# Optimization experiments

Hardware: AMD Instinct MI355X
Metric: run time of the kernel (lower is better)

Reference implementation:

```python
import jax, jax.numpy as jnp
import numpy as np
from jax import lax

B, T, D = 64, 1024, 256   # batch, seq_len, input_size
H, C = 1024, 1000         # hidden_size, num_classes


def setup_inputs() -> dict:
    key = jax.random.key(0)
    k_x, k_ih, k_hh, k_b, k_fc, k_fb = jax.random.split(key, 6)
    x = jax.random.normal(k_x, (B, T, D), dtype=jnp.float32)
    # scaled init so the 1024-step recurrence stays numerically sane
    w_ih = jax.random.normal(k_ih, (H, D), dtype=jnp.float32) * (1.0 / np.sqrt(D))
    w_hh = jax.random.normal(k_hh, (H, H), dtype=jnp.float32) * (0.5 / np.sqrt(H))
    b_mod = jax.random.normal(k_b, (H,), dtype=jnp.float32) * 0.01 - 0.1
    w_fc = jax.random.normal(k_fc, (C, H), dtype=jnp.float32) * (1.0 / np.sqrt(H))
    b_fc = jnp.zeros((C,), dtype=jnp.float32)
    return {"x": x, "w_ih": w_ih, "w_hh": w_hh, "b_mod": b_mod,
            "w_fc": w_fc, "b_fc": b_fc}


def reference(x, w_ih, w_hh, b_mod, w_fc, b_fc):
    # modReLU RNN: h_t = sign(z_t) * relu(|z_t| + b),  z_t = W_ih x_t + W_hh h_{t-1}
    # fc head applied to last hidden state (out[:, -1, :]).
    bsz = x.shape[0]
    # precompute input projections for all timesteps: [B, T, H]
    xproj = jnp.einsum('btd,hd->bth', x, w_ih)

    def step(h, x_t):
        z = x_t + h @ w_hh.T                      # [B, H]
        h_new = jnp.sign(z) * jnp.maximum(jnp.abs(z) + b_mod, 0.0)
        return h_new, None

    h0 = jnp.zeros((bsz, w_hh.shape[0]), dtype=x.dtype)
    h_last, _ = lax.scan(step, h0, jnp.swapaxes(xproj, 0, 1))  # scan over T
    return h_last @ w_fc.T + b_fc  # [B, C]
```

## Files before the change

kernel.cpp:

```cpp
#include <hip/hip_runtime.h>

typedef __bf16 bf16;
typedef __bf16 bf16x4 __attribute__((ext_vector_type(4)));
typedef __bf16 bf16x8 __attribute__((ext_vector_type(8)));
typedef float f32x4 __attribute__((ext_vector_type(4)));
typedef int   i32x4 __attribute__((ext_vector_type(4)));
typedef unsigned long long u64;
typedef unsigned int u32;

#define T_STEPS 1024
#define BATCH   64
#define DIN     256
#define HID     1024
#define NBLK    32
#define RING    8
#define SENT    0x7F7F7F7Fu

__global__ __launch_bounds__(256) void xproj_gemm(
    const float* __restrict__ x, const float* __restrict__ w_ih,
    bf16* __restrict__ xproj)
{
    __shared__ bf16 As[128 * 40];
    __shared__ bf16 Bs[128 * 40];
    const int tid = threadIdx.x;
    const int m0 = blockIdx.x * 128;
    const int n0 = blockIdx.y * 128;
    const int w = tid >> 6, lane = tid & 63;
    const int r = lane & 15, q = lane >> 4;

    f32x4 acc[2][8];
    #pragma unroll
    for (int i = 0; i < 2; i++)
        #pragma unroll
        for (int j = 0; j < 8; j++)
            acc[i][j] = (f32x4){0.f, 0.f, 0.f, 0.f};

    for (int kk = 0; kk < 8; kk++) {
        const int k0 = kk * 32;
        __syncthreads();
        #pragma unroll
        for (int j = 0; j < 4; j++) {
            int u = tid + j * 256;
            int row = u >> 3, c4 = u & 7;
            float4 fa = *(const float4*)&x[(size_t)(m0 + row) * DIN + k0 + c4 * 4];
            bf16x4 va = { (bf16)fa.x, (bf16)fa.y, (bf16)fa.z, (bf16)fa.w };
            *(bf16x4*)&As[row * 40 + c4 * 4] = va;
            float4 fb = *(const float4*)&w_ih[(size_t)(n0 + row) * DIN + k0 + c4 * 4];
            bf16x4 vb = { (bf16)fb.x, (bf16)fb.y, (bf16)fb.z, (bf16)fb.w };
            *(bf16x4*)&Bs[row * 40 + c4 * 4] = vb;
        }
        __syncthreads();
        bf16x8 a0 = *(const bf16x8*)&As[(w * 32 + r) * 40 + q * 8];
        bf16x8 a1 = *(const bf16x8*)&As[(w * 32 + 16 + r) * 40 + q * 8];
        #pragma unroll
        for (int nt = 0; nt < 8; nt++) {
            bf16x8 bb = *(const bf16x8*)&Bs[(nt * 16 + r) * 40 + q * 8];
            acc[0][nt] = __builtin_amdgcn_mfma_f32_16x16x32_bf16(a0, bb, acc[0][nt], 0, 0, 0);
            acc[1][nt] = __builtin_amdgcn_mfma_f32_16x16x32_bf16(a1, bb, acc[1][nt], 0, 0, 0);
        }
    }

    #pragma unroll
    for (int mi = 0; mi < 2; mi++)
        #pragma unroll
        for (int nt = 0; nt < 8; nt++)
            #pragma unroll
            for (int reg = 0; reg < 4; reg++) {
                int gm = m0 + w * 32 + mi * 16 + q * 4 + reg;
                int n  = n0 + nt * 16 + r;
                int b  = gm >> 10, t = gm & 1023;
                xproj[(((t << 6) + b) << 10) + n] = (bf16)acc[mi][nt][reg];
            }
}

__global__ __launch_bounds__(512, 2) void rnn_rec(
    const float* __restrict__ w_hh, const float* __restrict__ b_mod,
    const bf16* __restrict__ xproj, u64* __restrict__ hbuf,
    float* __restrict__ hT)
{
    __shared__ bf16 Wl[64 * 1032];
    __shared__ float Red[24 * 272];

    const int tid = threadIdx.x;
    const int fg2 = (int)(blockIdx.x >> 1);
    const int half = (int)(blockIdx.x & 1);
    const int f0 = fg2 * 64;
    const int b0 = half * 32;
    const int w = tid >> 6, lane = tid & 63;
    const int r = lane & 15, q = lane >> 4;
    const int bg = w & 1, kq = w >> 1;
    const int batchA = b0 + bg * 16 + r;

    for (int j = 0; j < 32; j++) {
        int u = tid + j * 512;
        int row = u >> 8, c4 = u & 255;
        float4 f = *(const float4*)&w_hh[(size_t)(f0 + row) * HID + c4 * 4];
        bf16x4 v = { (bf16)f.x, (bf16)f.y, (bf16)f.z, (bf16)f.w };
        *(bf16x4*)&Wl[row * 1032 + c4 * 4] = v;
    }
    const int myF = f0 + kq * 16 + r;
    const float bc = b_mod[myF];
    __syncthreads();

    bf16x8 Bf[4][8];
    #pragma unroll
    for (int nt = 0; nt < 4; nt++)
        #pragma unroll
        for (int ks = 0; ks < 8; ks++)
            Bf[nt][ks] = *(const bf16x8*)&Wl[(nt * 16 + r) * 1032 + kq * 256 + ks * 32 + q * 8];

    u32* hbuf32 = (u32*)hbuf;
    const size_t fragOff = (size_t)batchA * 2048 + kq * 512 + q * 16;

    float xpv[4];
    #pragma unroll
    for (int reg = 0; reg < 4; reg++) {
        int b = b0 + bg * 16 + q * 4 + reg;
        xpv[reg] = (float)xproj[(b << 10) + myF];
    }

    for (int t = 0; t < T_STEPS; t++) {
        const int rp = t & (RING - 1), wp = (t + 1) & (RING - 1);
        const char* Hb = (const char*)hbuf + (size_t)rp * 131072 + fragOff;

        union { i32x4 v[8]; u32 wd[32]; bf16x8 f[8]; } A;
        for (;;) {
            asm volatile(
                "global_load_dwordx4 %0, %8, off sc0 sc1\n\t"
                "global_load_dwordx4 %1, %8, off offset:64 sc0 sc1\n\t"
                "global_load_dwordx4 %2, %8, off offset:128 sc0 sc1\n\t"
                "global_load_dwordx4 %3, %8, off offset:192 sc0 sc1\n\t"
                "global_load_dwordx4 %4, %8, off offset:256 sc0 sc1\n\t"
                "global_load_dwordx4 %5, %8, off offset:320 sc0 sc1\n\t"
                "global_load_dwordx4 %6, %8, off offset:384 sc0 sc1\n\t"
                "global_load_dwordx4 %7, %8, off offset:448 sc0 sc1\n\t"
                "s_waitcnt vmcnt(0)"
                : "=v"(A.v[0]), "=v"(A.v[1]), "=v"(A.v[2]), "=v"(A.v[3]),
                  "=v"(A.v[4]), "=v"(A.v[5]), "=v"(A.v[6]), "=v"(A.v[7])
                : "v"(Hb)
                : "memory");
            bool ok = true;
            #pragma unroll
            for (int i = 0; i < 32; i++) ok &= (A.wd[i] != SENT);
            if (__all((int)ok)) break;
        }

        f32x4 acc[4];
        #pragma unroll
        for (int nt = 0; nt < 4; nt++) acc[nt] = (f32x4){0.f,0.f,0.f,0.f};
        #pragma unroll
        for (int ks = 0; ks < 8; ks++)
            #pragma unroll
            for (int nt = 0; nt < 4; nt++)
                acc[nt] = __builtin_amdgcn_mfma_f32_16x16x32_bf16(A.f[ks], Bf[nt][ks], acc[nt], 0, 0, 0);

        #pragma unroll
        for (int nt = 0; nt < 4; nt++) {
            if (nt == kq) continue;
            const int s = (kq - nt - 1) & 3;
            const int base = ((bg * 4 + nt) * 3 + s) * 272;
            #pragma unroll
            for (int reg = 0; reg < 4; reg++)
                Red[base + (q * 4 + reg) * 17 + r] = acc[nt][reg];
        }
        __syncthreads();

        float hv4[4];
        #pragma unroll
        for (int reg = 0; reg < 4; reg++) {
            float z = acc[kq][reg];
            #pragma unroll
            for (int s = 0; s < 3; s++)
                z += Red[((bg * 4 + kq) * 3 + s) * 272 + (q * 4 + reg) * 17 + r];
            z += xpv[reg];
            hv4[reg] = copysignf(fmaxf(fabsf(z) + bc, 0.0f), z);
        }
        __syncthreads();

        if (t == T_STEPS - 1) {
            #pragma unroll
            for (int reg = 0; reg < 4; reg++)
                hT[myF * 64 + b0 + bg * 16 + q * 4 + reg] = hv4[reg];
        } else {
            #pragma unroll
            for (int reg = 0; reg < 4; reg++) {
                const int b = b0 + bg * 16 + q * 4 + reg;
                float other = __shfl_xor(hv4[reg], 1);
                if ((r & 1) == 0) {
                    u32 lo = (u32)__builtin_bit_cast(unsigned short, (bf16)hv4[reg]);
                    u32 hi = (u32)__builtin_bit_cast(unsigned short, (bf16)other);
                    __hip_atomic_store(&hbuf32[(size_t)wp * 32768 + (b << 9) + (myF >> 1)],
                                       lo | (hi << 16), __ATOMIC_RELAXED, __HIP_MEMORY_SCOPE_AGENT);
                }
            }
            const size_t sp = (size_t)((t + 4) & (RING - 1)) * 32768;
            #pragma unroll
            for (int reg = 0; reg < 4; reg++) {
                const int b = b0 + bg * 16 + q * 4 + reg;
                if ((r & 1) == 0)
                    __hip_atomic_store(&hbuf32[sp + (b << 9) + (myF >> 1)],
                                       SENT, __ATOMIC_RELAXED, __HIP_MEMORY_SCOPE_AGENT);
            }
            #pragma unroll
            for (int reg = 0; reg < 4; reg++) {
                int b = b0 + bg * 16 + q * 4 + reg;
                xpv[reg] = (float)xproj[((size_t)(t + 1) << 16) + (b << 10) + myF];
            }
        }
    }
}

__global__ __launch_bounds__(256) void fc_head(
    const float* __restrict__ hT, const float* __restrict__ w_fc,
    const float* __restrict__ b_fc, float* __restrict__ out)
{
    const int tid = threadIdx.x;
    const int b = tid & 63;
    const int c = blockIdx.x * 4 + (tid >> 6);
    float acc = b_fc[c];
    #pragma unroll 8
    for (int k = 0; k < HID; k++)
        acc = fmaf(hT[k * 64 + b], w_fc[(size_t)c * HID + k], acc);
    out[b * 1000 + c] = acc;
}

extern "C" void kernel_launch(void* const* d_in, const int* in_sizes, int n_in,
                              void* d_out, int out_size, void* d_ws, size_t ws_size,
                              hipStream_t stream)
{
    const float* x     = (const float*)d_in[0];
    const float* w_ih  = (const float*)d_in[1];
    const float* w_hh  = (const float*)d_in[2];
    const float* b_mod = (const float*)d_in[3];
    const float* w_fc  = (const float*)d_in[4];
    const float* b_fc  = (const float*)d_in[5];
    float* out = (float*)d_out;

    char* ws = (char*)d_ws;
    bf16*  xproj = (bf16*)ws;
    u64*   hbuf  = (u64*)(ws + 134217728);
    float* hT    = (float*)(ws + 134217728 + 1048576);

    hipMemsetAsync(hbuf, 0, 131072, stream);
    hipMemsetAsync((char*)hbuf + 131072, 0x7F, 7 * 131072, stream);

    dim3 g1(512, 8);
    xproj_gemm<<<g1, 256, 0, stream>>>(x, w_ih, xproj);
    rnn_rec<<<NBLK, 512, 0, stream>>>(w_hh, b_mod, xproj, hbuf, hT);
    fc_head<<<250, 256, 0, stream>>>(hT, w_fc, b_fc, out);
}
```

Before: 5.022 ms.

## Split recurrence across 64 blocks with full-K per wave and per-chunk polling

The recurrent kernel now uses 64 blocks of 256 threads. Each block owns 64 features for one 16-batch group, and each wave holds the full K=1024 slice of W_hh in registers. This removes the cross-wave LDS reduction and both __syncthreads per timestep. The hidden-state polling becomes per-32-element chunk: MFMAs are issued as soon as each chunk's sentinel clears, instead of waiting for the whole fragment. The risks are heavy register pressure (32 B fragments plus 32 A buffers), twice as many blocks writing and spinning on the ring buffer, and extra loop overhead from the bitmask-guarded retries.

```diff
diff --git a/kernel.cpp b/kernel.cpp
--- a/kernel.cpp
+++ b/kernel.cpp
@@ -4,7 +4,6 @@
 typedef __bf16 bf16x4 __attribute__((ext_vector_type(4)));
 typedef __bf16 bf16x8 __attribute__((ext_vector_type(8)));
 typedef float f32x4 __attribute__((ext_vector_type(4)));
-typedef int   i32x4 __attribute__((ext_vector_type(4)));
 typedef unsigned long long u64;
 typedef unsigned int u32;
 
@@ -12,7 +11,7 @@
 #define BATCH   64
 #define DIN     256
 #define HID     1024
-#define NBLK    32
+#define NBLK    64
 #define RING    8
 #define SENT    0x7F7F7F7Fu
 
@@ -73,118 +72,96 @@
             }
 }
 
-__global__ __launch_bounds__(512, 2) void rnn_rec(
+__global__ __launch_bounds__(256, 1) void rnn_rec(
     const float* __restrict__ w_hh, const float* __restrict__ b_mod,
     const bf16* __restrict__ xproj, u64* __restrict__ hbuf,
     float* __restrict__ hT)
 {
     __shared__ bf16 Wl[64 * 1032];
-    __shared__ float Red[24 * 272];
 
     const int tid = threadIdx.x;
-    const int fg2 = (int)(blockIdx.x >> 1);
-    const int half = (int)(blockIdx.x & 1);
-    const int f0 = fg2 * 64;
-    const int b0 = half * 32;
+    const int fgq = (int)(blockIdx.x >> 2);
+    const int bg  = (int)(blockIdx.x & 3);
+    const int f0 = fgq * 64;
     const int w = tid >> 6, lane = tid & 63;
     const int r = lane & 15, q = lane >> 4;
-    const int bg = w & 1, kq = w >> 1;
-    const int batchA = b0 + bg * 16 + r;
-
-    for (int j = 0; j < 32; j++) {
-        int u = tid + j * 512;
+    const int myF = f0 + w * 16 + r;
+    const int batchA = bg * 16 + r;
+
+    for (int j = 0; j < 64; j++) {
+        int u = tid + j * 256;
         int row = u >> 8, c4 = u & 255;
         float4 f = *(const float4*)&w_hh[(size_t)(f0 + row) * HID + c4 * 4];
         bf16x4 v = { (bf16)f.x, (bf16)f.y, (bf16)f.z, (bf16)f.w };
         *(bf16x4*)&Wl[row * 1032 + c4 * 4] = v;
     }
-    const int myF = f0 + kq * 16 + r;
     const float bc = b_mod[myF];
     __syncthreads();
 
-    bf16x8 Bf[4][8];
-    #pragma unroll
-    for (int nt = 0; nt < 4; nt++)
-        #pragma unroll
-        for (int ks = 0; ks < 8; ks++)
-            Bf[nt][ks] = *(const bf16x8*)&Wl[(nt * 16 + r) * 1032 + kq * 256 + ks * 32 + q * 8];
+    bf16x8 Bf[32];
+    #pragma unroll
+    for (int ks = 0; ks < 32; ks++)
+        Bf[ks] = *(const bf16x8*)&Wl[(w * 16 + r) * 1032 + ks * 32 + q * 8];
 
     u32* hbuf32 = (u32*)hbuf;
-    const size_t fragOff = (size_t)batchA * 2048 + kq * 512 + q * 16;
 
     float xpv[4];
     #pragma unroll
     for (int reg = 0; reg < 4; reg++) {
-        int b = b0 + bg * 16 + q * 4 + reg;
+        int b = bg * 16 + q * 4 + reg;
         xpv[reg] = (float)xproj[(b << 10) + myF];
     }
 
     for (int t = 0; t < T_STEPS; t++) {
         const int rp = t & (RING - 1), wp = (t + 1) & (RING - 1);
-        const char* Hb = (const char*)hbuf + (size_t)rp * 131072 + fragOff;
-
-        union { i32x4 v[8]; u32 wd[32]; bf16x8 f[8]; } A;
-        for (;;) {
-            asm volatile(
-                "global_load_dwordx4 %0, %8, off sc0 sc1\n\t"
-                "global_load_dwordx4 %1, %8, off offset:64 sc0 sc1\n\t"
-                "global_load_dwordx4 %2, %8, off offset:128 sc0 sc1\n\t"
-                "global_load_dwordx4 %3, %8, off offset:192 sc0 sc1\n\t"
-                "global_load_dwordx4 %4, %8, off offset:256 sc0 sc1\n\t"
-                "global_load_dwordx4 %5, %8, off offset:320 sc0 sc1\n\t"
-                "global_load_dwordx4 %6, %8, off offset:384 sc0 sc1\n\t"
-                "global_load_dwordx4 %7, %8, off offset:448 sc0 sc1\n\t"
-                "s_waitcnt vmcnt(0)"
-                : "=v"(A.v[0]), "=v"(A.v[1]), "=v"(A.v[2]), "=v"(A.v[3]),
-                  "=v"(A.v[4]), "=v"(A.v[5]), "=v"(A.v[6]), "=v"(A.v[7])
-                : "v"(Hb)
-                : "memory");
-            bool ok = true;
-            #pragma unroll
-            for (int i = 0; i < 32; i++) ok &= (A.wd[i] != SENT);
-            if (__all((int)ok)) break;
-        }
-
-        f32x4 acc[4];
-        #pragma unroll
-        for (int nt = 0; nt < 4; nt++) acc[nt] = (f32x4){0.f,0.f,0.f,0.f};
-        #pragma unroll
-        for (int ks = 0; ks < 8; ks++)
-            #pragma unroll
-            for (int nt = 0; nt < 4; nt++)
-                acc[nt] = __builtin_amdgcn_mfma_f32_16x16x32_bf16(A.f[ks], Bf[nt][ks], acc[nt], 0, 0, 0);
-
-        #pragma unroll
-        for (int nt = 0; nt < 4; nt++) {
-            if (nt == kq) continue;
-            const int s = (kq - nt - 1) & 3;
-            const int base = ((bg * 4 + nt) * 3 + s) * 272;
+        const u64* H = hbuf + (size_t)rp * 16384 + (size_t)batchA * 256 + q * 2;
+
+        union { u64 u[2]; u32 wd[4]; bf16x8 f; } A[32];
+        f32x4 acc0 = {0.f,0.f,0.f,0.f}, acc1 = {0.f,0.f,0.f,0.f};
+        f32x4 acc2 = {0.f,0.f,0.f,0.f}, acc3 = {0.f,0.f,0.f,0.f};
+        u32 pend = 0xFFFFFFFFu;
+        while (pend) {
+            #pragma unroll
+            for (int ks = 0; ks < 32; ks++) {
+                if (pend & (1u << ks)) {
+                    A[ks].u[0] = __hip_atomic_load(&H[ks * 8    ], __ATOMIC_RELAXED, __HIP_MEMORY_SCOPE_AGENT);
+                    A[ks].u[1] = __hip_atomic_load(&H[ks * 8 + 1], __ATOMIC_RELAXED, __HIP_MEMORY_SCOPE_AGENT);
+                }
+            }
+            #pragma unroll
+            for (int ks = 0; ks < 32; ks++) {
+                if (pend & (1u << ks)) {
+                    bool ok = (A[ks].wd[0] != SENT) & (A[ks].wd[1] != SENT)
+                            & (A[ks].wd[2] != SENT) & (A[ks].wd[3] != SENT);
+                    if (__all((int)ok)) {
+                        switch (ks & 3) {
+                            case 0: acc0 = __builtin_amdgcn_mfma_f32_16x16x32_bf16(A[ks].f, Bf[ks], acc0, 0, 0, 0); break;
+                            case 1: acc1 = __builtin_amdgcn_mfma_f32_16x16x32_bf16(A[ks].f, Bf[ks], acc1, 0, 0, 0); break;
+                            case 2: acc2 = __builtin_amdgcn_mfma_f32_16x16x32_bf16(A[ks].f, Bf[ks], acc2, 0, 0, 0); break;
+                            default: acc3 = __builtin_amdgcn_mfma_f32_16x16x32_bf16(A[ks].f, Bf[ks], acc3, 0, 0, 0); break;
+                        }
+                        pend &= ~(1u << ks);
+                    }
+                }
+            }
+        }
+
+        f32x4 zs = (acc0 + acc1) + (acc2 + acc3);
+        float hv4[4];
+        #pragma unroll
+        for (int reg = 0; reg < 4; reg++) {
+            float z = zs[reg] + xpv[reg];
+            hv4[reg] = copysignf(fmaxf(fabsf(z) + bc, 0.0f), z);
+        }
+
+        if (t == T_STEPS - 1) {
             #pragma unroll
             for (int reg = 0; reg < 4; reg++)
-                Red[base + (q * 4 + reg) * 17 + r] = acc[nt][reg];
-        }
-        __syncthreads();
-
-        float hv4[4];
-        #pragma unroll
-        for (int reg = 0; reg < 4; reg++) {
-            float z = acc[kq][reg];
-            #pragma unroll
-            for (int s = 0; s < 3; s++)
-                z += Red[((bg * 4 + kq) * 3 + s) * 272 + (q * 4 + reg) * 17 + r];
-            z += xpv[reg];
-            hv4[reg] = copysignf(fmaxf(fabsf(z) + bc, 0.0f), z);
-        }
-        __syncthreads();
-
-        if (t == T_STEPS - 1) {
-            #pragma unroll
-            for (int reg = 0; reg < 4; reg++)
-                hT[myF * 64 + b0 + bg * 16 + q * 4 + reg] = hv4[reg];
+                hT[myF * 64 + bg * 16 + q * 4 + reg] = hv4[reg];
         } else {
             #pragma unroll
             for (int reg = 0; reg < 4; reg++) {
-                const int b = b0 + bg * 16 + q * 4 + reg;
+                const int b = bg * 16 + q * 4 + reg;
                 float other = __shfl_xor(hv4[reg], 1);
                 if ((r & 1) == 0) {
                     u32 lo = (u32)__builtin_bit_cast(unsigned short, (bf16)hv4[reg]);
@@ -196,14 +173,14 @@
             const size_t sp = (size_t)((t + 4) & (RING - 1)) * 32768;
             #pragma unroll
             for (int reg = 0; reg < 4; reg++) {
-                const int b = b0 + bg * 16 + q * 4 + reg;
+                const int b = bg * 16 + q * 4 + reg;
                 if ((r & 1) == 0)
                     __hip_atomic_store(&hbuf32[sp + (b << 9) + (myF >> 1)],
                                        SENT, __ATOMIC_RELAXED, __HIP_MEMORY_SCOPE_AGENT);
             }
             #pragma unroll
             for (int reg = 0; reg < 4; reg++) {
-                int b = b0 + bg * 16 + q * 4 + reg;
+                int b = bg * 16 + q * 4 + reg;
                 xpv[reg] = (float)xproj[((size_t)(t + 1) << 16) + (b << 10) + myF];
             }
         }
@@ -246,6 +223,6 @@
 
     dim3 g1(512, 8);
     xproj_gemm<<<g1, 256, 0, stream>>>(x, w_ih, xproj);
-    rnn_rec<<<NBLK, 512, 0, stream>>>(w_hh, b_mod, xproj, hbuf, hT);
+    rnn_rec<<<NBLK, 256, 0, stream>>>(w_hh, b_mod, xproj, hbuf, hT);
     fc_head<<<250, 256, 0, stream>>>(hT, w_fc, b_fc, out);
 }
```

After: 11.26 ms. +124.2%, slower.
